# Kernel optimization log

Hardware: AMD Instinct MI355X
Metric: run time of the kernel (lower is better)

Reference implementation:

```python
import jax, jax.numpy as jnp
import numpy as np

D_MODEL = 256
NHEAD = 8
D_HEAD = D_MODEL // NHEAD


def setup_inputs() -> dict:
    key = jax.random.key(0)
    ks = jax.random.split(key, 5)
    s = 0.02
    return {
        "x": jax.random.normal(ks[0], (2, 4096, D_MODEL), dtype=jnp.float32),
        "source": jax.random.normal(ks[1], (2, 6144, D_MODEL), dtype=jnp.float32),
        "Wq": jax.random.normal(ks[2], (D_MODEL, D_MODEL), dtype=jnp.float32) * s,
        "Wk": jax.random.normal(ks[3], (D_MODEL, D_MODEL), dtype=jnp.float32) * s,
        "Wv": jax.random.normal(ks[4], (D_MODEL, D_MODEL), dtype=jnp.float32) * s,
    }


def reference(x, source, Wq, Wk, Wv):
    B, L1, D = x.shape
    L2 = source.shape[1]
    scale = D_HEAD ** (-0.5)
    # torch Linear: y = x @ W.T  (W is [out, in])
    q = (x @ Wq.T).reshape(B, L1, NHEAD, D_HEAD)
    k = (source @ Wk.T).reshape(B, L2, NHEAD, D_HEAD)
    v = (source @ Wv.T).reshape(B, L2, NHEAD, D_HEAD)
    # scores: [B, H, L1, L2]
    attn = jnp.einsum("bqhd,bkhd->bhqk", q, k) * scale
    attn = jax.nn.softmax(attn, axis=-1)
    out = jnp.einsum("bhqk,bkhd->bqhd", attn, v)
    return out.reshape(B, L1, D)
```

## Files before the change

### kernel.cpp

```cpp
#include <hip/hip_runtime.h>
#include <math.h>

#define B_   2
#define L1_  4096
#define L2_  6144
#define DM_  256
#define H_   8
#define DH_  32

typedef __bf16 bf16x8 __attribute__((ext_vector_type(8)));
typedef __bf16 bf16x4 __attribute__((ext_vector_type(4)));
typedef float floatx4 __attribute__((ext_vector_type(4)));
typedef _Float16 f16;
typedef _Float16 f16x4 __attribute__((ext_vector_type(4)));
typedef _Float16 f16x8 __attribute__((ext_vector_type(8)));
typedef __fp16 fp16v2 __attribute__((ext_vector_type(2)));

__device__ __forceinline__ bf16x8 ldb(const __bf16* p) { return *(const bf16x8*)p; }

__device__ __forceinline__ bf16x4 pack4(floatx4 v) {
    bf16x4 r;
    r[0] = (__bf16)v[0]; r[1] = (__bf16)v[1];
    r[2] = (__bf16)v[2]; r[3] = (__bf16)v[3];
    return r;
}

__device__ __forceinline__ float pkrtz(float a, float b) {
    fp16v2 p = __builtin_amdgcn_cvt_pkrtz(a, b);
    return __builtin_bit_cast(float, p);
}

__global__ __launch_bounds__(256) void cvt_all(
    const float* __restrict__ wq, const float* __restrict__ wk,
    const float* __restrict__ wv, const float* __restrict__ x,
    const float* __restrict__ src,
    __bf16* __restrict__ wbf, __bf16* __restrict__ xbf, __bf16* __restrict__ sbf,
    float qscale)
{
    int i = blockIdx.x * 256 + threadIdx.x;
    const float* s; __bf16* d; float sc = 1.0f; size_t off;
    if (i < 49152) {
        int seg = i >> 14;
        off = (size_t)(i & 16383) * 4;
        s = seg == 0 ? wq : (seg == 1 ? wk : wv);
        d = wbf + (size_t)seg * 65536;
        if (seg == 0) sc = qscale;
    } else if (i < 49152 + 524288) {
        off = (size_t)(i - 49152) * 4; s = x; d = xbf;
    } else {
        off = (size_t)(i - 49152 - 524288) * 4; s = src; d = sbf;
    }
    float4 v = *(const float4*)(s + off);
    bf16x4 r;
    r[0] = (__bf16)(v.x * sc); r[1] = (__bf16)(v.y * sc);
    r[2] = (__bf16)(v.z * sc); r[3] = (__bf16)(v.w * sc);
    *(bf16x4*)(d + off) = r;
}

__global__ __launch_bounds__(256) void proj_kernel(
    const __bf16* __restrict__ xbf, const __bf16* __restrict__ sbf,
    const __bf16* __restrict__ Wbf,
    __bf16* __restrict__ qo, __bf16* __restrict__ ko, f16* __restrict__ vo)
{
    __shared__ f16 ldsV[256 * 36];

    const int bid = blockIdx.x;
    int y, xb;
    if      (bid < 256) { y = 0; xb = bid; }
    else if (bid < 640) { y = 1; xb = bid - 256; }
    else                { y = 2; xb = bid - 640; }

    const int L = (y == 0) ? L1_ : L2_;
    const __bf16* X   = (y == 0) ? xbf : sbf;
    const __bf16* Wb  = Wbf + (size_t)y * 65536;

    const int lane = threadIdx.x & 63;
    const int w    = threadIdx.x >> 6;
    const int g    = lane >> 4;
    const int c    = lane & 15;
    const int mb   = xb * 32;
    const int b    = mb / L;
    const int lb   = mb - b * L;

    floatx4 acc[2][4];
#pragma unroll
    for (int s = 0; s < 2; s++)
#pragma unroll
        for (int n = 0; n < 4; n++) acc[s][n] = (floatx4){0.f, 0.f, 0.f, 0.f};

#pragma unroll
    for (int kc = 0; kc < 8; kc++) {
        bf16x8 xf0 = ldb(X + (size_t)(mb + c) * DM_ + kc * 32 + g * 8);
        bf16x8 xf1 = ldb(X + (size_t)(mb + 16 + c) * DM_ + kc * 32 + g * 8);
#pragma unroll
        for (int n = 0; n < 4; n++) {
            const int oc = w * 64 + n * 16 + c;
            bf16x8 wf = ldb(Wb + (size_t)oc * DM_ + kc * 32 + g * 8);
            if (y == 2) {
                acc[0][n] = __builtin_amdgcn_mfma_f32_16x16x32_bf16(xf0, wf, acc[0][n], 0, 0, 0);
                acc[1][n] = __builtin_amdgcn_mfma_f32_16x16x32_bf16(xf1, wf, acc[1][n], 0, 0, 0);
            } else {
                acc[0][n] = __builtin_amdgcn_mfma_f32_16x16x32_bf16(wf, xf0, acc[0][n], 0, 0, 0);
                acc[1][n] = __builtin_amdgcn_mfma_f32_16x16x32_bf16(wf, xf1, acc[1][n], 0, 0, 0);
            }
        }
    }

    const int bhb = b * H_;
    if (y == 2) {
#pragma unroll
        for (int s = 0; s < 2; s++)
#pragma unroll
            for (int n = 0; n < 4; n++) {
                int dg = w * 64 + (n >> 1) * 32 + (n & 1) * 16 + c;
                int ll = s * 16 + g * 4;
                float2 pr;
                pr.x = pkrtz(acc[s][n][0], acc[s][n][1]);
                pr.y = pkrtz(acc[s][n][2], acc[s][n][3]);
                *(float2*)(ldsV + (size_t)dg * 36 + ll) = pr;
            }
        __syncthreads();
        const int t = threadIdx.x;
        const int h = t >> 5, d = t & 31;
        f16* row = vo + ((size_t)(bhb + h) * DH_ + d) * (size_t)L + lb;
#pragma unroll
        for (int j = 0; j < 8; j++)
            *(f16x4*)(row + j * 4) = *(const f16x4*)(ldsV + (size_t)t * 36 + j * 4);
    } else {
        __bf16* out = (y == 0) ? qo : ko;
#pragma unroll
        for (int s = 0; s < 2; s++)
#pragma unroll
            for (int n = 0; n < 4; n++) {
                int dlo = (n & 1) * 16 + g * 4;
                int h = w * 2 + (n >> 1);
                int l = lb + s * 16 + c;
                *(bf16x4*)(out + ((size_t)(bhb + h) * (size_t)L + l) * DH_ + dlo) = pack4(acc[s][n]);
            }
    }
}

__device__ __forceinline__ void attn_step(
    const bf16x8 (&qf)[4], const bf16x8 (&kf)[4], bf16x8 (&kfN)[4],
    const __bf16* __restrict__ knext,
    const f16* __restrict__ vb0, const f16* __restrict__ vb1, int kb,
    f16* __restrict__ Pw, int g, int c,
    float (&l)[4], floatx4 (&o)[4][2])
{
    f16x8 vf[4];
    vf[0] = *(const f16x8*)(vb0 + kb);
    vf[1] = *(const f16x8*)(vb1 + kb);
    vf[2] = *(const f16x8*)(vb0 + kb + 32);
    vf[3] = *(const f16x8*)(vb1 + kb + 32);
    kfN[0] = ldb(knext);
    kfN[1] = ldb(knext + 16 * DH_);
    kfN[2] = ldb(knext + 32 * DH_);
    kfN[3] = ldb(knext + 48 * DH_);

#pragma unroll
    for (int hp = 0; hp < 2; hp++) {
#pragma unroll
        for (int hh = 0; hh < 2; hh++) {
            const int h = hp * 2 + hh;
            floatx4 s[4];
#pragma unroll
            for (int st = 0; st < 4; st++)
                s[st] = __builtin_amdgcn_mfma_f32_16x16x32_bf16(
                            kf[st], qf[h], (floatx4){0.f, 0.f, 0.f, 0.f}, 0, 0, 0);
#pragma unroll
            for (int st = 0; st < 4; st++) {
                float e0 = __builtin_amdgcn_exp2f(s[st][0]);
                float e1 = __builtin_amdgcn_exp2f(s[st][1]);
                float e2 = __builtin_amdgcn_exp2f(s[st][2]);
                float e3 = __builtin_amdgcn_exp2f(s[st][3]);
                l[h] += (e0 + e1) + (e2 + e3);
                float2 pr;
                pr.x = pkrtz(e0, e1);
                pr.y = pkrtz(e2, e3);
                *(float2*)(Pw + hh * 1024 + ((st * 2 + (g >> 1)) * 16 + c) * 8 + (g & 1) * 4) = pr;
            }
        }
#pragma unroll
        for (int kc = 0; kc < 2; kc++)
#pragma unroll
            for (int hh = 0; hh < 2; hh++) {
                const int h = hp * 2 + hh;
                f16x8 pa = *(const f16x8*)(Pw + hh * 1024 + ((kc * 4 + g) * 16 + c) * 8);
                o[h][0] = __builtin_amdgcn_mfma_f32_16x16x32_f16(pa, vf[kc * 2 + 0], o[h][0], 0, 0, 0);
                o[h][1] = __builtin_amdgcn_mfma_f32_16x16x32_f16(pa, vf[kc * 2 + 1], o[h][1], 0, 0, 0);
            }
    }
}

template<bool DIRECT>
__global__ __launch_bounds__(256, 2) void attn_kernel(
    const __bf16* __restrict__ Q, const __bf16* __restrict__ K,
    const f16* __restrict__ VT, float* __restrict__ out,
    f16* __restrict__ Opart, float* __restrict__ Lpart, int klen, int split)
{
    __shared__ f16 ldsP[4][2][1024];

    const int bid  = blockIdx.x;
    const int work = (bid & 7) * (32 * split) + (bid >> 3);
    const int xb   = work & 15;
    const int bh   = (work >> 4) & 15;
    const int z    = work >> 8;

    const int lane  = threadIdx.x & 63;
    const int w     = threadIdx.x >> 6;
    const int g     = lane >> 4;
    const int c     = lane & 15;
    const int qbase = xb * 256 + w * 64;
    const int k0    = z * klen;

    bf16x8 qf[4];
#pragma unroll
    for (int h = 0; h < 4; h++)
        qf[h] = ldb(Q + ((size_t)bh * L1_ + qbase + h * 16 + c) * DH_ + g * 8);

    const __bf16* kbase = K  + (size_t)bh * L2_ * DH_ + (size_t)c * DH_ + g * 8;
    const f16*    vb0   = VT + ((size_t)bh * DH_ + c)      * L2_ + g * 8;
    const f16*    vb1   = VT + ((size_t)bh * DH_ + 16 + c) * L2_ + g * 8;
    f16* Pw = &ldsP[w][0][0];

    float l[4] = {0.f, 0.f, 0.f, 0.f};
    floatx4 o[4][2];
#pragma unroll
    for (int h = 0; h < 4; h++) { o[h][0] = (floatx4){0.f,0.f,0.f,0.f}; o[h][1] = (floatx4){0.f,0.f,0.f,0.f}; }

    bf16x8 kfA[4], kfB[4];
#pragma unroll
    for (int st = 0; st < 4; st++)
        kfA[st] = ldb(kbase + (size_t)(k0 + st * 16) * DH_);

    for (int t = 0; t < klen; t += 128) {
        int kb = k0 + t;
        attn_step(qf, kfA, kfB, kbase + (size_t)(kb + 64) * DH_,
                  vb0, vb1, kb, Pw, g, c, l, o);
        int nn = (t + 128 < klen) ? kb + 128 : k0;
        attn_step(qf, kfB, kfA, kbase + (size_t)nn * DH_,
                  vb0, vb1, kb + 64, Pw, g, c, l, o);
    }

#pragma unroll
    for (int h = 0; h < 4; h++) {
        l[h] += __shfl_xor(l[h], 16, 64);
        l[h] += __shfl_xor(l[h], 32, 64);
    }

    const int b  = bh / H_;
    const int hh = bh % H_;
    if (DIRECT) {
#pragma unroll
        for (int h = 0; h < 4; h++)
#pragma unroll
            for (int r = 0; r < 4; r++) {
                float lr  = __shfl(l[h], g * 4 + r, 64);
                float inv = 1.0f / lr;
                size_t base = ((size_t)(b * L1_ + qbase + h * 16 + g * 4 + r)) * DM_ + hh * DH_;
                out[base + c]      = o[h][0][r] * inv;
                out[base + 16 + c] = o[h][1][r] * inv;
            }
    } else {
        f16* Op = Opart + (size_t)z * ((size_t)B_ * L1_ * DM_);
#pragma unroll
        for (int h = 0; h < 4; h++) {
#pragma unroll
            for (int r = 0; r < 4; r++) {
                size_t base = ((size_t)(b * L1_ + qbase + h * 16 + g * 4 + r)) * DM_ + hh * DH_;
                Op[base + c]      = (f16)o[h][0][r];
                Op[base + 16 + c] = (f16)o[h][1][r];
            }
            if (g == 0)
                Lpart[(size_t)z * ((size_t)B_ * H_ * L1_) +
                      (size_t)bh * L1_ + qbase + h * 16 + c] = l[h];
        }
    }
}

__global__ __launch_bounds__(256) void combine_kernel(
    const f16* __restrict__ Opart, const float* __restrict__ Lpart,
    float* __restrict__ out, int split)
{
    int t   = blockIdx.x * 256 + threadIdx.x;
    int row = t >> 6;
    int col = (t & 63) * 4;
    int b   = row >> 12;
    int q   = row & (L1_ - 1);
    int bh  = b * H_ + (col >> 5);
    float4 a = {0.f, 0.f, 0.f, 0.f};
    float ls = 0.f;
    for (int z = 0; z < split; z++) {
        const f16* Op = Opart + (size_t)z * ((size_t)B_ * L1_ * DM_);
        f16x4 v = *(const f16x4*)(Op + (size_t)row * DM_ + col);
        a.x += (float)v[0]; a.y += (float)v[1];
        a.z += (float)v[2]; a.w += (float)v[3];
        ls += Lpart[(size_t)z * ((size_t)B_ * H_ * L1_) + (size_t)bh * L1_ + q];
    }
    float inv = 1.0f / ls;
    float4 r; r.x = a.x * inv; r.y = a.y * inv; r.z = a.z * inv; r.w = a.w * inv;
    *(float4*)(out + (size_t)row * DM_ + col) = r;
}

extern "C" void kernel_launch(void* const* d_in, const int* in_sizes, int n_in,
                              void* d_out, int out_size, void* d_ws, size_t ws_size,
                              hipStream_t stream) {
    const float* x   = (const float*)d_in[0];
    const float* src = (const float*)d_in[1];
    const float* Wq  = (const float*)d_in[2];
    const float* Wk  = (const float*)d_in[3];
    const float* Wv  = (const float*)d_in[4];
    float* out = (float*)d_out;

    const float qscale = 1.4426950408889634f / sqrtf((float)DH_);

    const size_t nW = 3 * 65536;
    const size_t nQ = (size_t)B_ * H_ * L1_ * DH_;
    const size_t nK = (size_t)B_ * H_ * L2_ * DH_;
    const size_t nX = nQ;

    __bf16* wbf = (__bf16*)d_ws;
    __bf16* qws = wbf + nW;
    __bf16* kws = qws + nQ;
    f16*    vt  = (f16*)(kws + nK);
    size_t unionOff = ((nW + nQ + 2 * nK) * 2 + 255) & ~(size_t)255;
    __bf16* xbf = (__bf16*)((char*)d_ws + unionOff);
    __bf16* sbf = xbf + nX;

    const size_t oPartB = (size_t)B_ * L1_ * DM_ * sizeof(f16);
    const size_t lPartB = (size_t)B_ * H_ * L1_ * 4;
    const size_t avail  = ws_size > unionOff ? ws_size - unionOff : 0;
    int split = 1;
    if      (avail >= 8 * (oPartB + lPartB)) split = 8;
    else if (avail >= 6 * (oPartB + lPartB)) split = 6;
    else if (avail >= 4 * (oPartB + lPartB)) split = 4;
    else if (avail >= 2 * (oPartB + lPartB)) split = 2;
    f16*   Opart = (f16*)((char*)d_ws + unionOff);
    float* Lpart = (float*)((char*)d_ws + unionOff + (size_t)split * oPartB);

    cvt_all<<<dim3(5312), 256, 0, stream>>>(Wq, Wk, Wv, x, src, wbf, xbf, sbf, qscale);
    proj_kernel<<<dim3(1024), 256, 0, stream>>>(xbf, sbf, wbf, qws, kws, vt);

    if (split > 1) {
        attn_kernel<false><<<dim3(256 * split), 256, 0, stream>>>(
            qws, kws, vt, nullptr, Opart, Lpart, L2_ / split, split);
        combine_kernel<<<dim3(2048), 256, 0, stream>>>(Opart, Lpart, out, split);
    } else {
        attn_kernel<true><<<dim3(256), 256, 0, stream>>>(
            qws, kws, vt, out, nullptr, nullptr, L2_, 1);
    }
}
```

Before: 188.8 us.

## Fuse activation conversion into projection and shrink attention tiles for occupancy

The standalone fp32-to-bf16 conversion of x and source is removed, and the projection kernel now loads fp32 activations and converts them in registers, using 16-row tiles across twice as many blocks. The attention kernel drops the double-buffered K prefetch and processes 2 query subtiles per wave instead of 4, with half the LDS, so it can declare 4 blocks per CU instead of 2. The split-6 option is also removed. The aim is to save a full activation round-trip through memory and gain occupancy to hide latency, at the cost of losing explicit K prefetch and re-reading K/V for twice as many query blocks.

```diff
diff --git a/kernel.cpp b/kernel.cpp
--- a/kernel.cpp
+++ b/kernel.cpp
@@ -30,138 +30,153 @@
     return __builtin_bit_cast(float, p);
 }
 
-__global__ __launch_bounds__(256) void cvt_all(
+__device__ __forceinline__ bf16x8 loadx8(const float* __restrict__ p) {
+    float4 a = *(const float4*)p;
+    float4 b = *(const float4*)(p + 4);
+    bf16x8 r;
+    r[0] = (__bf16)a.x; r[1] = (__bf16)a.y; r[2] = (__bf16)a.z; r[3] = (__bf16)a.w;
+    r[4] = (__bf16)b.x; r[5] = (__bf16)b.y; r[6] = (__bf16)b.z; r[7] = (__bf16)b.w;
+    return r;
+}
+
+__global__ __launch_bounds__(256) void cvtW_kernel(
     const float* __restrict__ wq, const float* __restrict__ wk,
-    const float* __restrict__ wv, const float* __restrict__ x,
-    const float* __restrict__ src,
-    __bf16* __restrict__ wbf, __bf16* __restrict__ xbf, __bf16* __restrict__ sbf,
-    float qscale)
+    const float* __restrict__ wv, __bf16* __restrict__ o, float qscale)
 {
     int i = blockIdx.x * 256 + threadIdx.x;
-    const float* s; __bf16* d; float sc = 1.0f; size_t off;
-    if (i < 49152) {
-        int seg = i >> 14;
-        off = (size_t)(i & 16383) * 4;
-        s = seg == 0 ? wq : (seg == 1 ? wk : wv);
-        d = wbf + (size_t)seg * 65536;
-        if (seg == 0) sc = qscale;
-    } else if (i < 49152 + 524288) {
-        off = (size_t)(i - 49152) * 4; s = x; d = xbf;
-    } else {
-        off = (size_t)(i - 49152 - 524288) * 4; s = src; d = sbf;
-    }
-    float4 v = *(const float4*)(s + off);
+    int seg = i >> 14;
+    int off = (i & 16383) * 4;
+    const float* src = seg == 0 ? wq : (seg == 1 ? wk : wv);
+    float s = seg == 0 ? qscale : 1.0f;
+    float4 v = *(const float4*)(src + off);
+    __bf16* dst = o + (size_t)seg * 65536 + off;
     bf16x4 r;
-    r[0] = (__bf16)(v.x * sc); r[1] = (__bf16)(v.y * sc);
-    r[2] = (__bf16)(v.z * sc); r[3] = (__bf16)(v.w * sc);
-    *(bf16x4*)(d + off) = r;
+    r[0] = (__bf16)(v.x * s); r[1] = (__bf16)(v.y * s);
+    r[2] = (__bf16)(v.z * s); r[3] = (__bf16)(v.w * s);
+    *(bf16x4*)(dst + 0) = r;
 }
 
 __global__ __launch_bounds__(256) void proj_kernel(
-    const __bf16* __restrict__ xbf, const __bf16* __restrict__ sbf,
+    const float* __restrict__ x, const float* __restrict__ src,
     const __bf16* __restrict__ Wbf,
     __bf16* __restrict__ qo, __bf16* __restrict__ ko, f16* __restrict__ vo)
 {
-    __shared__ f16 ldsV[256 * 36];
+    __shared__ f16 ldsV[256 * 24];
 
     const int bid = blockIdx.x;
     int y, xb;
-    if      (bid < 256) { y = 0; xb = bid; }
-    else if (bid < 640) { y = 1; xb = bid - 256; }
-    else                { y = 2; xb = bid - 640; }
+    if      (bid < 512)  { y = 0; xb = bid; }
+    else if (bid < 1280) { y = 1; xb = bid - 512; }
+    else                 { y = 2; xb = bid - 1280; }
 
     const int L = (y == 0) ? L1_ : L2_;
-    const __bf16* X   = (y == 0) ? xbf : sbf;
-    const __bf16* Wb  = Wbf + (size_t)y * 65536;
+    const float*  X  = (y == 0) ? x : src;
+    const __bf16* Wb = Wbf + (size_t)y * 65536;
 
     const int lane = threadIdx.x & 63;
     const int w    = threadIdx.x >> 6;
     const int g    = lane >> 4;
     const int c    = lane & 15;
-    const int mb   = xb * 32;
+    const int mb   = xb * 16;
     const int b    = mb / L;
     const int lb   = mb - b * L;
 
-    floatx4 acc[2][4];
-#pragma unroll
-    for (int s = 0; s < 2; s++)
-#pragma unroll
-        for (int n = 0; n < 4; n++) acc[s][n] = (floatx4){0.f, 0.f, 0.f, 0.f};
+    floatx4 acc[4];
+#pragma unroll
+    for (int n = 0; n < 4; n++) acc[n] = (floatx4){0.f, 0.f, 0.f, 0.f};
 
 #pragma unroll
     for (int kc = 0; kc < 8; kc++) {
-        bf16x8 xf0 = ldb(X + (size_t)(mb + c) * DM_ + kc * 32 + g * 8);
-        bf16x8 xf1 = ldb(X + (size_t)(mb + 16 + c) * DM_ + kc * 32 + g * 8);
+        bf16x8 xf = loadx8(X + (size_t)(mb + c) * DM_ + kc * 32 + g * 8);
 #pragma unroll
         for (int n = 0; n < 4; n++) {
             const int oc = w * 64 + n * 16 + c;
             bf16x8 wf = ldb(Wb + (size_t)oc * DM_ + kc * 32 + g * 8);
-            if (y == 2) {
-                acc[0][n] = __builtin_amdgcn_mfma_f32_16x16x32_bf16(xf0, wf, acc[0][n], 0, 0, 0);
-                acc[1][n] = __builtin_amdgcn_mfma_f32_16x16x32_bf16(xf1, wf, acc[1][n], 0, 0, 0);
-            } else {
-                acc[0][n] = __builtin_amdgcn_mfma_f32_16x16x32_bf16(wf, xf0, acc[0][n], 0, 0, 0);
-                acc[1][n] = __builtin_amdgcn_mfma_f32_16x16x32_bf16(wf, xf1, acc[1][n], 0, 0, 0);
-            }
+            if (y == 2)
+                acc[n] = __builtin_amdgcn_mfma_f32_16x16x32_bf16(xf, wf, acc[n], 0, 0, 0);
+            else
+                acc[n] = __builtin_amdgcn_mfma_f32_16x16x32_bf16(wf, xf, acc[n], 0, 0, 0);
         }
     }
 
     const int bhb = b * H_;
     if (y == 2) {
 #pragma unroll
-        for (int s = 0; s < 2; s++)
-#pragma unroll
-            for (int n = 0; n < 4; n++) {
-                int dg = w * 64 + (n >> 1) * 32 + (n & 1) * 16 + c;
-                int ll = s * 16 + g * 4;
-                float2 pr;
-                pr.x = pkrtz(acc[s][n][0], acc[s][n][1]);
-                pr.y = pkrtz(acc[s][n][2], acc[s][n][3]);
-                *(float2*)(ldsV + (size_t)dg * 36 + ll) = pr;
-            }
+        for (int n = 0; n < 4; n++) {
+            int oc = w * 64 + n * 16 + c;
+            float2 pr;
+            pr.x = pkrtz(acc[n][0], acc[n][1]);
+            pr.y = pkrtz(acc[n][2], acc[n][3]);
+            *(float2*)(ldsV + (size_t)oc * 24 + g * 4) = pr;
+        }
         __syncthreads();
         const int t = threadIdx.x;
-        const int h = t >> 5, d = t & 31;
-        f16* row = vo + ((size_t)(bhb + h) * DH_ + d) * (size_t)L + lb;
-#pragma unroll
-        for (int j = 0; j < 8; j++)
-            *(f16x4*)(row + j * 4) = *(const f16x4*)(ldsV + (size_t)t * 36 + j * 4);
+        f16* row = vo + ((size_t)(bhb + (t >> 5)) * DH_ + (t & 31)) * (size_t)L + lb;
+        *(f16x8*)(row)     = *(const f16x8*)(ldsV + (size_t)t * 24);
+        *(f16x8*)(row + 8) = *(const f16x8*)(ldsV + (size_t)t * 24 + 8);
     } else {
         __bf16* out = (y == 0) ? qo : ko;
 #pragma unroll
-        for (int s = 0; s < 2; s++)
-#pragma unroll
-            for (int n = 0; n < 4; n++) {
-                int dlo = (n & 1) * 16 + g * 4;
-                int h = w * 2 + (n >> 1);
-                int l = lb + s * 16 + c;
-                *(bf16x4*)(out + ((size_t)(bhb + h) * (size_t)L + l) * DH_ + dlo) = pack4(acc[s][n]);
-            }
-    }
-}
-
-__device__ __forceinline__ void attn_step(
-    const bf16x8 (&qf)[4], const bf16x8 (&kf)[4], bf16x8 (&kfN)[4],
-    const __bf16* __restrict__ knext,
-    const f16* __restrict__ vb0, const f16* __restrict__ vb1, int kb,
-    f16* __restrict__ Pw, int g, int c,
-    float (&l)[4], floatx4 (&o)[4][2])
+        for (int n = 0; n < 4; n++) {
+            int dlo = (n & 1) * 16 + g * 4;
+            int h = w * 2 + (n >> 1);
+            int l = lb + c;
+            *(bf16x4*)(out + ((size_t)(bhb + h) * (size_t)L + l) * DH_ + dlo) = pack4(acc[n]);
+        }
+    }
+}
+
+template<bool DIRECT>
+__global__ __launch_bounds__(256, 4) void attn_kernel(
+    const __bf16* __restrict__ Q, const __bf16* __restrict__ K,
+    const f16* __restrict__ VT, float* __restrict__ out,
+    f16* __restrict__ Opart, float* __restrict__ Lpart, int klen, int split)
 {
-    f16x8 vf[4];
-    vf[0] = *(const f16x8*)(vb0 + kb);
-    vf[1] = *(const f16x8*)(vb1 + kb);
-    vf[2] = *(const f16x8*)(vb0 + kb + 32);
-    vf[3] = *(const f16x8*)(vb1 + kb + 32);
-    kfN[0] = ldb(knext);
-    kfN[1] = ldb(knext + 16 * DH_);
-    kfN[2] = ldb(knext + 32 * DH_);
-    kfN[3] = ldb(knext + 48 * DH_);
-
-#pragma unroll
-    for (int hp = 0; hp < 2; hp++) {
-#pragma unroll
-        for (int hh = 0; hh < 2; hh++) {
-            const int h = hp * 2 + hh;
+    __shared__ f16 ldsP[4][1024];
+
+    const int bid  = blockIdx.x;
+    const int work = (bid & 7) * (64 * split) + (bid >> 3);
+    const int xb   = work & 31;
+    const int bh   = (work >> 5) & 15;
+    const int z    = work >> 9;
+
+    const int lane  = threadIdx.x & 63;
+    const int w     = threadIdx.x >> 6;
+    const int g     = lane >> 4;
+    const int c     = lane & 15;
+    const int qbase = xb * 128 + w * 32;
+    const int k0    = z * klen;
+
+    bf16x8 qf[2];
+#pragma unroll
+    for (int h = 0; h < 2; h++)
+        qf[h] = ldb(Q + ((size_t)bh * L1_ + qbase + h * 16 + c) * DH_ + g * 8);
+
+    const __bf16* kbase = K  + (size_t)bh * L2_ * DH_ + (size_t)c * DH_ + g * 8;
+    const f16*    vb0   = VT + ((size_t)bh * DH_ + c)      * L2_ + g * 8;
+    const f16*    vb1   = VT + ((size_t)bh * DH_ + 16 + c) * L2_ + g * 8;
+    f16* Pw = &ldsP[w][0];
+
+    float l[2] = {0.f, 0.f};
+    floatx4 o[2][2];
+#pragma unroll
+    for (int h = 0; h < 2; h++) { o[h][0] = (floatx4){0.f,0.f,0.f,0.f}; o[h][1] = (floatx4){0.f,0.f,0.f,0.f}; }
+
+    for (int t = 0; t < klen; t += 64) {
+        const int kb = k0 + t;
+        bf16x8 kf[4];
+        kf[0] = ldb(kbase + (size_t)kb * DH_);
+        kf[1] = ldb(kbase + (size_t)(kb + 16) * DH_);
+        kf[2] = ldb(kbase + (size_t)(kb + 32) * DH_);
+        kf[3] = ldb(kbase + (size_t)(kb + 48) * DH_);
+        f16x8 vf[4];
+        vf[0] = *(const f16x8*)(vb0 + kb);
+        vf[1] = *(const f16x8*)(vb1 + kb);
+        vf[2] = *(const f16x8*)(vb0 + kb + 32);
+        vf[3] = *(const f16x8*)(vb1 + kb + 32);
+
+#pragma unroll
+        for (int h = 0; h < 2; h++) {
             floatx4 s[4];
 #pragma unroll
             for (int st = 0; st < 4; st++)
@@ -177,73 +192,19 @@
                 float2 pr;
                 pr.x = pkrtz(e0, e1);
                 pr.y = pkrtz(e2, e3);
-                *(float2*)(Pw + hh * 1024 + ((st * 2 + (g >> 1)) * 16 + c) * 8 + (g & 1) * 4) = pr;
+                *(float2*)(Pw + ((st * 2 + (g >> 1)) * 16 + c) * 8 + (g & 1) * 4) = pr;
             }
-        }
-#pragma unroll
-        for (int kc = 0; kc < 2; kc++)
-#pragma unroll
-            for (int hh = 0; hh < 2; hh++) {
-                const int h = hp * 2 + hh;
-                f16x8 pa = *(const f16x8*)(Pw + hh * 1024 + ((kc * 4 + g) * 16 + c) * 8);
+#pragma unroll
+            for (int kc = 0; kc < 2; kc++) {
+                f16x8 pa = *(const f16x8*)(Pw + ((kc * 4 + g) * 16 + c) * 8);
                 o[h][0] = __builtin_amdgcn_mfma_f32_16x16x32_f16(pa, vf[kc * 2 + 0], o[h][0], 0, 0, 0);
                 o[h][1] = __builtin_amdgcn_mfma_f32_16x16x32_f16(pa, vf[kc * 2 + 1], o[h][1], 0, 0, 0);
             }
-    }
-}
-
-template<bool DIRECT>
-__global__ __launch_bounds__(256, 2) void attn_kernel(
-    const __bf16* __restrict__ Q, const __bf16* __restrict__ K,
-    const f16* __restrict__ VT, float* __restrict__ out,
-    f16* __restrict__ Opart, float* __restrict__ Lpart, int klen, int split)
-{
-    __shared__ f16 ldsP[4][2][1024];
-
-    const int bid  = blockIdx.x;
-    const int work = (bid & 7) * (32 * split) + (bid >> 3);
-    const int xb   = work & 15;
-    const int bh   = (work >> 4) & 15;
-    const int z    = work >> 8;
-
-    const int lane  = threadIdx.x & 63;
-    const int w     = threadIdx.x >> 6;
-    const int g     = lane >> 4;
-    const int c     = lane & 15;
-    const int qbase = xb * 256 + w * 64;
-    const int k0    = z * klen;
-
-    bf16x8 qf[4];
-#pragma unroll
-    for (int h = 0; h < 4; h++)
-        qf[h] = ldb(Q + ((size_t)bh * L1_ + qbase + h * 16 + c) * DH_ + g * 8);
-
-    const __bf16* kbase = K  + (size_t)bh * L2_ * DH_ + (size_t)c * DH_ + g * 8;
-    const f16*    vb0   = VT + ((size_t)bh * DH_ + c)      * L2_ + g * 8;
-    const f16*    vb1   = VT + ((size_t)bh * DH_ + 16 + c) * L2_ + g * 8;
-    f16* Pw = &ldsP[w][0][0];
-
-    float l[4] = {0.f, 0.f, 0.f, 0.f};
-    floatx4 o[4][2];
-#pragma unroll
-    for (int h = 0; h < 4; h++) { o[h][0] = (floatx4){0.f,0.f,0.f,0.f}; o[h][1] = (floatx4){0.f,0.f,0.f,0.f}; }
-
-    bf16x8 kfA[4], kfB[4];
-#pragma unroll
-    for (int st = 0; st < 4; st++)
-        kfA[st] = ldb(kbase + (size_t)(k0 + st * 16) * DH_);
-
-    for (int t = 0; t < klen; t += 128) {
-        int kb = k0 + t;
-        attn_step(qf, kfA, kfB, kbase + (size_t)(kb + 64) * DH_,
-                  vb0, vb1, kb, Pw, g, c, l, o);
-        int nn = (t + 128 < klen) ? kb + 128 : k0;
-        attn_step(qf, kfB, kfA, kbase + (size_t)nn * DH_,
-                  vb0, vb1, kb + 64, Pw, g, c, l, o);
-    }
-
-#pragma unroll
-    for (int h = 0; h < 4; h++) {
+        }
+    }
+
+#pragma unroll
+    for (int h = 0; h < 2; h++) {
         l[h] += __shfl_xor(l[h], 16, 64);
         l[h] += __shfl_xor(l[h], 32, 64);
     }
@@ -252,7 +213,7 @@
     const int hh = bh % H_;
     if (DIRECT) {
 #pragma unroll
-        for (int h = 0; h < 4; h++)
+        for (int h = 0; h < 2; h++)
 #pragma unroll
             for (int r = 0; r < 4; r++) {
                 float lr  = __shfl(l[h], g * 4 + r, 64);
@@ -264,7 +225,7 @@
     } else {
         f16* Op = Opart + (size_t)z * ((size_t)B_ * L1_ * DM_);
 #pragma unroll
-        for (int h = 0; h < 4; h++) {
+        for (int h = 0; h < 2; h++) {
 #pragma unroll
             for (int r = 0; r < 4; r++) {
                 size_t base = ((size_t)(b * L1_ + qbase + h * 16 + g * 4 + r)) * DM_ + hh * DH_;
@@ -317,36 +278,32 @@
     const size_t nW = 3 * 65536;
     const size_t nQ = (size_t)B_ * H_ * L1_ * DH_;
     const size_t nK = (size_t)B_ * H_ * L2_ * DH_;
-    const size_t nX = nQ;
 
     __bf16* wbf = (__bf16*)d_ws;
     __bf16* qws = wbf + nW;
     __bf16* kws = qws + nQ;
     f16*    vt  = (f16*)(kws + nK);
-    size_t unionOff = ((nW + nQ + 2 * nK) * 2 + 255) & ~(size_t)255;
-    __bf16* xbf = (__bf16*)((char*)d_ws + unionOff);
-    __bf16* sbf = xbf + nX;
+    size_t tailOff = ((nW + nQ + 2 * nK) * 2 + 255) & ~(size_t)255;
 
     const size_t oPartB = (size_t)B_ * L1_ * DM_ * sizeof(f16);
     const size_t lPartB = (size_t)B_ * H_ * L1_ * 4;
-    const size_t avail  = ws_size > unionOff ? ws_size - unionOff : 0;
+    const size_t avail  = ws_size > tailOff ? ws_size - tailOff : 0;
     int split = 1;
     if      (avail >= 8 * (oPartB + lPartB)) split = 8;
-    else if (avail >= 6 * (oPartB + lPartB)) split = 6;
     else if (avail >= 4 * (oPartB + lPartB)) split = 4;
     else if (avail >= 2 * (oPartB + lPartB)) split = 2;
-    f16*   Opart = (f16*)((char*)d_ws + unionOff);
-    float* Lpart = (float*)((char*)d_ws + unionOff + (size_t)split * oPartB);
-
-    cvt_all<<<dim3(5312), 256, 0, stream>>>(Wq, Wk, Wv, x, src, wbf, xbf, sbf, qscale);
-    proj_kernel<<<dim3(1024), 256, 0, stream>>>(xbf, sbf, wbf, qws, kws, vt);
+    f16*   Opart = (f16*)((char*)d_ws + tailOff);
+    float* Lpart = (float*)((char*)d_ws + tailOff + (size_t)split * oPartB);
+
+    cvtW_kernel<<<dim3(192), 256, 0, stream>>>(Wq, Wk, Wv, wbf, qscale);
+    proj_kernel<<<dim3(2048), 256, 0, stream>>>(x, src, wbf, qws, kws, vt);
 
     if (split > 1) {
-        attn_kernel<false><<<dim3(256 * split), 256, 0, stream>>>(
+        attn_kernel<false><<<dim3(512 * split), 256, 0, stream>>>(
             qws, kws, vt, nullptr, Opart, Lpart, L2_ / split, split);
         combine_kernel<<<dim3(2048), 256, 0, stream>>>(Opart, Lpart, out, split);
     } else {
-        attn_kernel<true><<<dim3(256), 256, 0, stream>>>(
+        attn_kernel<true><<<dim3(512), 256, 0, stream>>>(
             qws, kws, vt, out, nullptr, nullptr, L2_, 1);
     }
 }
```

After: 262.8 us. 39.2% more time.

## Fuse activation fp32-to-bf16 conversion into projection and widen memory accesses

Applied to the files above, without the earlier changes.

The conversion kernel now handles only the weights, and the projection kernel reads fp32 x/source directly and converts them in registers. This removes a full write and re-read of the bf16 activation copies. Several unrelated tweaks ride along: wider V-transpose stores and combine loads/stores, split row-sum accumulators in attention to shorten the dependency chain, launch bounds raised to 3 blocks per SM, and split=6 dropped. The higher occupancy target may force register spills, and the projection kernel now moves twice as many activation bytes per load.

```diff
diff --git a/kernel.cpp b/kernel.cpp
--- a/kernel.cpp
+++ b/kernel.cpp
@@ -30,35 +30,34 @@
     return __builtin_bit_cast(float, p);
 }
 
-__global__ __launch_bounds__(256) void cvt_all(
+__device__ __forceinline__ bf16x8 loadx8(const float* __restrict__ p) {
+    float4 a = *(const float4*)p;
+    float4 b = *(const float4*)(p + 4);
+    bf16x8 r;
+    r[0] = (__bf16)a.x; r[1] = (__bf16)a.y; r[2] = (__bf16)a.z; r[3] = (__bf16)a.w;
+    r[4] = (__bf16)b.x; r[5] = (__bf16)b.y; r[6] = (__bf16)b.z; r[7] = (__bf16)b.w;
+    return r;
+}
+
+__global__ __launch_bounds__(256) void cvtW_kernel(
     const float* __restrict__ wq, const float* __restrict__ wk,
-    const float* __restrict__ wv, const float* __restrict__ x,
-    const float* __restrict__ src,
-    __bf16* __restrict__ wbf, __bf16* __restrict__ xbf, __bf16* __restrict__ sbf,
-    float qscale)
+    const float* __restrict__ wv, __bf16* __restrict__ o, float qscale)
 {
     int i = blockIdx.x * 256 + threadIdx.x;
-    const float* s; __bf16* d; float sc = 1.0f; size_t off;
-    if (i < 49152) {
-        int seg = i >> 14;
-        off = (size_t)(i & 16383) * 4;
-        s = seg == 0 ? wq : (seg == 1 ? wk : wv);
-        d = wbf + (size_t)seg * 65536;
-        if (seg == 0) sc = qscale;
-    } else if (i < 49152 + 524288) {
-        off = (size_t)(i - 49152) * 4; s = x; d = xbf;
-    } else {
-        off = (size_t)(i - 49152 - 524288) * 4; s = src; d = sbf;
-    }
-    float4 v = *(const float4*)(s + off);
+    int seg = i >> 14;
+    int off = (i & 16383) * 4;
+    const float* src = seg == 0 ? wq : (seg == 1 ? wk : wv);
+    float s = seg == 0 ? qscale : 1.0f;
+    float4 v = *(const float4*)(src + off);
+    __bf16* dst = o + (size_t)seg * 65536 + off;
     bf16x4 r;
-    r[0] = (__bf16)(v.x * sc); r[1] = (__bf16)(v.y * sc);
-    r[2] = (__bf16)(v.z * sc); r[3] = (__bf16)(v.w * sc);
-    *(bf16x4*)(d + off) = r;
+    r[0] = (__bf16)(v.x * s); r[1] = (__bf16)(v.y * s);
+    r[2] = (__bf16)(v.z * s); r[3] = (__bf16)(v.w * s);
+    *(bf16x4*)dst = r;
 }
 
 __global__ __launch_bounds__(256) void proj_kernel(
-    const __bf16* __restrict__ xbf, const __bf16* __restrict__ sbf,
+    const float* __restrict__ x, const float* __restrict__ src,
     const __bf16* __restrict__ Wbf,
     __bf16* __restrict__ qo, __bf16* __restrict__ ko, f16* __restrict__ vo)
 {
@@ -71,8 +70,8 @@
     else                { y = 2; xb = bid - 640; }
 
     const int L = (y == 0) ? L1_ : L2_;
-    const __bf16* X   = (y == 0) ? xbf : sbf;
-    const __bf16* Wb  = Wbf + (size_t)y * 65536;
+    const float*  X  = (y == 0) ? x : src;
+    const __bf16* Wb = Wbf + (size_t)y * 65536;
 
     const int lane = threadIdx.x & 63;
     const int w    = threadIdx.x >> 6;
@@ -90,8 +89,8 @@
 
 #pragma unroll
     for (int kc = 0; kc < 8; kc++) {
-        bf16x8 xf0 = ldb(X + (size_t)(mb + c) * DM_ + kc * 32 + g * 8);
-        bf16x8 xf1 = ldb(X + (size_t)(mb + 16 + c) * DM_ + kc * 32 + g * 8);
+        bf16x8 xf0 = loadx8(X + (size_t)(mb + c) * DM_ + kc * 32 + g * 8);
+        bf16x8 xf1 = loadx8(X + (size_t)(mb + 16 + c) * DM_ + kc * 32 + g * 8);
 #pragma unroll
         for (int n = 0; n < 4; n++) {
             const int oc = w * 64 + n * 16 + c;
@@ -121,11 +120,10 @@
             }
         __syncthreads();
         const int t = threadIdx.x;
-        const int h = t >> 5, d = t & 31;
-        f16* row = vo + ((size_t)(bhb + h) * DH_ + d) * (size_t)L + lb;
-#pragma unroll
-        for (int j = 0; j < 8; j++)
-            *(f16x4*)(row + j * 4) = *(const f16x4*)(ldsV + (size_t)t * 36 + j * 4);
+        f16* row = vo + ((size_t)(bhb + (t >> 5)) * DH_ + (t & 31)) * (size_t)L + lb;
+#pragma unroll
+        for (int j = 0; j < 4; j++)
+            *(f16x8*)(row + j * 8) = *(const f16x8*)(ldsV + (size_t)t * 36 + j * 8);
     } else {
         __bf16* out = (y == 0) ? qo : ko;
 #pragma unroll
@@ -145,7 +143,7 @@
     const __bf16* __restrict__ knext,
     const f16* __restrict__ vb0, const f16* __restrict__ vb1, int kb,
     f16* __restrict__ Pw, int g, int c,
-    float (&l)[4], floatx4 (&o)[4][2])
+    float (&la)[4], float (&lb_)[4], floatx4 (&o)[4][2])
 {
     f16x8 vf[4];
     vf[0] = *(const f16x8*)(vb0 + kb);
@@ -173,7 +171,8 @@
                 float e1 = __builtin_amdgcn_exp2f(s[st][1]);
                 float e2 = __builtin_amdgcn_exp2f(s[st][2]);
                 float e3 = __builtin_amdgcn_exp2f(s[st][3]);
-                l[h] += (e0 + e1) + (e2 + e3);
+                if (st < 2) la[h]  += (e0 + e1) + (e2 + e3);
+                else        lb_[h] += (e0 + e1) + (e2 + e3);
                 float2 pr;
                 pr.x = pkrtz(e0, e1);
                 pr.y = pkrtz(e2, e3);
@@ -193,7 +192,7 @@
 }
 
 template<bool DIRECT>
-__global__ __launch_bounds__(256, 2) void attn_kernel(
+__global__ __launch_bounds__(256, 3) void attn_kernel(
     const __bf16* __restrict__ Q, const __bf16* __restrict__ K,
     const f16* __restrict__ VT, float* __restrict__ out,
     f16* __restrict__ Opart, float* __restrict__ Lpart, int klen, int split)
@@ -223,7 +222,7 @@
     const f16*    vb1   = VT + ((size_t)bh * DH_ + 16 + c) * L2_ + g * 8;
     f16* Pw = &ldsP[w][0][0];
 
-    float l[4] = {0.f, 0.f, 0.f, 0.f};
+    float la[4] = {0.f, 0.f, 0.f, 0.f}, lb_[4] = {0.f, 0.f, 0.f, 0.f};
     floatx4 o[4][2];
 #pragma unroll
     for (int h = 0; h < 4; h++) { o[h][0] = (floatx4){0.f,0.f,0.f,0.f}; o[h][1] = (floatx4){0.f,0.f,0.f,0.f}; }
@@ -236,14 +235,16 @@
     for (int t = 0; t < klen; t += 128) {
         int kb = k0 + t;
         attn_step(qf, kfA, kfB, kbase + (size_t)(kb + 64) * DH_,
-                  vb0, vb1, kb, Pw, g, c, l, o);
+                  vb0, vb1, kb, Pw, g, c, la, lb_, o);
         int nn = (t + 128 < klen) ? kb + 128 : k0;
         attn_step(qf, kfB, kfA, kbase + (size_t)nn * DH_,
-                  vb0, vb1, kb + 64, Pw, g, c, l, o);
-    }
-
+                  vb0, vb1, kb + 64, Pw, g, c, la, lb_, o);
+    }
+
+    float l[4];
 #pragma unroll
     for (int h = 0; h < 4; h++) {
+        l[h] = la[h] + lb_[h];
         l[h] += __shfl_xor(l[h], 16, 64);
         l[h] += __shfl_xor(l[h], 32, 64);
     }
@@ -283,23 +284,26 @@
     float* __restrict__ out, int split)
 {
     int t   = blockIdx.x * 256 + threadIdx.x;
-    int row = t >> 6;
-    int col = (t & 63) * 4;
+    int row = t >> 5;
+    int col = (t & 31) * 8;
     int b   = row >> 12;
     int q   = row & (L1_ - 1);
     int bh  = b * H_ + (col >> 5);
-    float4 a = {0.f, 0.f, 0.f, 0.f};
+    float a[8] = {0.f,0.f,0.f,0.f,0.f,0.f,0.f,0.f};
     float ls = 0.f;
     for (int z = 0; z < split; z++) {
         const f16* Op = Opart + (size_t)z * ((size_t)B_ * L1_ * DM_);
-        f16x4 v = *(const f16x4*)(Op + (size_t)row * DM_ + col);
-        a.x += (float)v[0]; a.y += (float)v[1];
-        a.z += (float)v[2]; a.w += (float)v[3];
+        f16x8 v = *(const f16x8*)(Op + (size_t)row * DM_ + col);
+#pragma unroll
+        for (int j = 0; j < 8; j++) a[j] += (float)v[j];
         ls += Lpart[(size_t)z * ((size_t)B_ * H_ * L1_) + (size_t)bh * L1_ + q];
     }
     float inv = 1.0f / ls;
-    float4 r; r.x = a.x * inv; r.y = a.y * inv; r.z = a.z * inv; r.w = a.w * inv;
-    *(float4*)(out + (size_t)row * DM_ + col) = r;
+    float4 r0, r1;
+    r0.x = a[0]*inv; r0.y = a[1]*inv; r0.z = a[2]*inv; r0.w = a[3]*inv;
+    r1.x = a[4]*inv; r1.y = a[5]*inv; r1.z = a[6]*inv; r1.w = a[7]*inv;
+    *(float4*)(out + (size_t)row * DM_ + col)     = r0;
+    *(float4*)(out + (size_t)row * DM_ + col + 4) = r1;
 }
 
 extern "C" void kernel_launch(void* const* d_in, const int* in_sizes, int n_in,
@@ -317,34 +321,30 @@
     const size_t nW = 3 * 65536;
     const size_t nQ = (size_t)B_ * H_ * L1_ * DH_;
     const size_t nK = (size_t)B_ * H_ * L2_ * DH_;
-    const size_t nX = nQ;
 
     __bf16* wbf = (__bf16*)d_ws;
     __bf16* qws = wbf + nW;
     __bf16* kws = qws + nQ;
     f16*    vt  = (f16*)(kws + nK);
-    size_t unionOff = ((nW + nQ + 2 * nK) * 2 + 255) & ~(size_t)255;
-    __bf16* xbf = (__bf16*)((char*)d_ws + unionOff);
-    __bf16* sbf = xbf + nX;
+    size_t tailOff = ((nW + nQ + 2 * nK) * 2 + 255) & ~(size_t)255;
 
     const size_t oPartB = (size_t)B_ * L1_ * DM_ * sizeof(f16);
     const size_t lPartB = (size_t)B_ * H_ * L1_ * 4;
-    const size_t avail  = ws_size > unionOff ? ws_size - unionOff : 0;
+    const size_t avail  = ws_size > tailOff ? ws_size - tailOff : 0;
     int split = 1;
     if      (avail >= 8 * (oPartB + lPartB)) split = 8;
-    else if (avail >= 6 * (oPartB + lPartB)) split = 6;
     else if (avail >= 4 * (oPartB + lPartB)) split = 4;
     else if (avail >= 2 * (oPartB + lPartB)) split = 2;
-    f16*   Opart = (f16*)((char*)d_ws + unionOff);
-    float* Lpart = (float*)((char*)d_ws + unionOff + (size_t)split * oPartB);
-
-    cvt_all<<<dim3(5312), 256, 0, stream>>>(Wq, Wk, Wv, x, src, wbf, xbf, sbf, qscale);
-    proj_kernel<<<dim3(1024), 256, 0, stream>>>(xbf, sbf, wbf, qws, kws, vt);
+    f16*   Opart = (f16*)((char*)d_ws + tailOff);
+    float* Lpart = (float*)((char*)d_ws + tailOff + (size_t)split * oPartB);
+
+    cvtW_kernel<<<dim3(192), 256, 0, stream>>>(Wq, Wk, Wv, wbf, qscale);
+    proj_kernel<<<dim3(1024), 256, 0, stream>>>(x, src, wbf, qws, kws, vt);
 
     if (split > 1) {
         attn_kernel<false><<<dim3(256 * split), 256, 0, stream>>>(
             qws, kws, vt, nullptr, Opart, Lpart, L2_ / split, split);
-        combine_kernel<<<dim3(2048), 256, 0, stream>>>(Opart, Lpart, out, split);
+        combine_kernel<<<dim3(1024), 256, 0, stream>>>(Opart, Lpart, out, split);
     } else {
         attn_kernel<true><<<dim3(256), 256, 0, stream>>>(
             qws, kws, vt, out, nullptr, nullptr, L2_, 1);
```

Result: slower. 258.5 us (+36.9%).
